# Performance work log

Hardware: AMD Instinct MI355X
Metric: run time of the kernel (lower is better)

The kernel has to match this reference:

```python
import jax, jax.numpy as jnp
import numpy as np

B, S, D, H, FF = 4, 2048, 512, 8, 2048
W = 128  # local attention window size (hardcoded in module)
DH = D // H


def _ln(x, g, b, eps=1e-5):
    m = x.mean(-1, keepdims=True)
    v = ((x - m) ** 2).mean(-1, keepdims=True)
    return (x - m) / jnp.sqrt(v + eps) * g + b


def setup_inputs() -> dict:
    key = jax.random.key(0)
    ks = jax.random.split(key, 10)
    s = 0.02
    return {
        "src": jax.random.normal(ks[0], (B, S, D), jnp.float32),
        # global nn.MultiheadAttention params
        "in_proj_w": jax.random.normal(ks[1], (3 * D, D), jnp.float32) * s,
        "in_proj_b": jnp.zeros((3 * D,), jnp.float32),
        "out_proj_w": jax.random.normal(ks[2], (D, D), jnp.float32) * s,
        "out_proj_b": jnp.zeros((D,), jnp.float32),
        # LocalMHA params (prenorm LN, fused qkv no-bias, out proj no-bias)
        "ln_g": jnp.ones((D,), jnp.float32),
        "ln_b": jnp.zeros((D,), jnp.float32),
        "qkv_w": jax.random.normal(ks[3], (3 * D, D), jnp.float32) * s,
        "to_out_w": jax.random.normal(ks[4], (D, D), jnp.float32) * s,
        # glFusion + FFN + norms
        "gl_w": jax.random.normal(ks[5], (D, 2 * D), jnp.float32) * s,
        "gl_b": jnp.zeros((D,), jnp.float32),
        "norm1_g": jnp.ones((D,), jnp.float32),
        "norm1_b": jnp.zeros((D,), jnp.float32),
        "lin1_w": jax.random.normal(ks[6], (FF, D), jnp.float32) * s,
        "lin1_b": jnp.zeros((FF,), jnp.float32),
        "lin2_w": jax.random.normal(ks[7], (D, FF), jnp.float32) * s,
        "lin2_b": jnp.zeros((D,), jnp.float32),
        "norm2_g": jnp.ones((D,), jnp.float32),
        "norm2_b": jnp.zeros((D,), jnp.float32),
    }


def _forward(src, in_proj_w, in_proj_b, out_proj_w, out_proj_b, ln_g, ln_b,
             qkv_w, to_out_w, gl_w, gl_b, norm1_g, norm1_b,
             lin1_w, lin1_b, lin2_w, lin2_b, norm2_g, norm2_b):
    b, s, d = src.shape
    scale = DH ** -0.5

    def heads(x):  # (b, s, d) -> (b, H, s, DH)
        return x.reshape(b, s, H, DH).transpose(0, 2, 1, 3)

    # ---- global full MHA (no mask) ----
    qkv = src @ in_proj_w.T + in_proj_b
    qg, kg, vg = (heads(t) for t in jnp.split(qkv, 3, axis=-1))
    att = jax.nn.softmax(jnp.einsum('bhid,bhjd->bhij', qg, kg) * scale, axis=-1)
    go = jnp.einsum('bhij,bhjd->bhid', att, vg).transpose(0, 2, 1, 3).reshape(b, s, d)
    go = go @ out_proj_w.T + out_proj_b

    # ---- local windowed causal MHA with rotary (window=128, look_backward=1) ----
    x = _ln(src, ln_g, ln_b)  # prenorm
    ql, kl, vl = (heads(t) for t in jnp.split(x @ qkv_w.T, 3, axis=-1))

    pos = jnp.arange(s)
    inv_freq = 1.0 / (10000.0 ** (jnp.arange(0, DH, 2, dtype=jnp.float32) / DH))
    freqs = pos[:, None].astype(jnp.float32) * inv_freq[None, :]
    emb = jnp.concatenate([freqs, freqs], axis=-1)  # (s, DH)
    cos, sin = jnp.cos(emb), jnp.sin(emb)

    def rope(t):
        h = DH // 2
        t1, t2 = t[..., :h], t[..., h:]
        return t * cos + jnp.concatenate([-t2, t1], axis=-1) * sin

    ql, kl = rope(ql), rope(kl)
    ql = ql * scale

    nw = s // W
    qw = ql.reshape(b, H, nw, W, DH)
    kw = kl.reshape(b, H, nw, W, DH)
    vw = vl.reshape(b, H, nw, W, DH)

    def look_back(t):  # concat previous window with current: (b,H,nw,2W,DH)
        prev = jnp.pad(t, ((0, 0), (0, 0), (1, 0), (0, 0), (0, 0)))[:, :, :-1]
        return jnp.concatenate([prev, t], axis=3)

    bk, bv = look_back(kw), look_back(vw)

    qpos = pos.reshape(nw, W)
    kpos = jnp.concatenate(
        [jnp.concatenate([jnp.full((1, W), -1, pos.dtype), qpos[:-1]], axis=0), qpos],
        axis=1)  # (nw, 2W)
    mask = (kpos[:, None, :] >= 0) & (kpos[:, None, :] <= qpos[:, :, None])  # (nw,W,2W)

    sc = jnp.einsum('bhnid,bhnjd->bhnij', qw, bk)
    sc = jnp.where(mask, sc, jnp.finfo(sc.dtype).min)
    at = jax.nn.softmax(sc, axis=-1)
    lo = jnp.einsum('bhnij,bhnjd->bhnid', at, bv).reshape(b, H, s, DH)
    lo = lo.transpose(0, 2, 1, 3).reshape(b, s, d) @ to_out_w.T

    # ---- fuse global+local, residual, norms, FFN ----
    src2 = jnp.concatenate([go, lo], axis=-1) @ gl_w.T + gl_b
    h1 = _ln(src + src2, norm1_g, norm1_b)
    ff = jax.nn.relu(h1 @ lin1_w.T + lin1_b) @ lin2_w.T + lin2_b
    return _ln(h1 + ff, norm2_g, norm2_b)


def reference(src, in_proj_w, in_proj_b, out_proj_w, out_proj_b, ln_g, ln_b,
              qkv_w, to_out_w, gl_w, gl_b, norm1_g, norm1_b,
              lin1_w, lin1_b, lin2_w, lin2_b, norm2_g, norm2_b):
    return _forward(src, in_proj_w, in_proj_b, out_proj_w, out_proj_b, ln_g, ln_b,
                    qkv_w, to_out_w, gl_w, gl_b, norm1_g, norm1_b,
                    lin1_w, lin1_b, lin2_w, lin2_b, norm2_g, norm2_b)
```

## Files before the change

### kernel.cpp

```cpp
#include <hip/hip_runtime.h>
#include <math.h>

#define B_  4
#define S_  2048
#define D_  512
#define H_  8
#define FF_ 2048
#define W_  128
#define DH_ 64
#define TRD (3*D_)
#define MR_ (B_*S_)
#define LDO_ 1024

typedef __attribute__((ext_vector_type(8)))  short short8;
typedef __attribute__((ext_vector_type(4)))  float f32x4;
typedef __attribute__((ext_vector_type(16))) float f32x16;

__device__ __forceinline__ short f2bf(float f) {
    unsigned u = __float_as_uint(f);
    unsigned r = (u + 0x7fff + ((u >> 16) & 1)) >> 16;
    return (short)r;
}
__device__ __forceinline__ float bf2f(ushort u) {
    return __uint_as_float(((unsigned)u) << 16);
}
__device__ __forceinline__ unsigned pack_bf_trunc(float f0, float f1) {
    return __builtin_amdgcn_perm(__float_as_uint(f1), __float_as_uint(f0), 0x07060302u);
}
__device__ __forceinline__ void gload_lds16(const ushort* g, short* l) {
    __builtin_amdgcn_global_load_lds(
        (const __attribute__((address_space(1))) void*)g,
        (__attribute__((address_space(3))) void*)l, 16, 0, 0);
}

struct CvtJobs { const float* s[8]; ushort* d[8]; int n[8]; };

__global__ __launch_bounds__(256) void cvt_kernel(CvtJobs jobs)
{
    int i4 = (blockIdx.x * 256 + threadIdx.x) * 4;
    #pragma unroll
    for (int j = 0; j < 8; j++) {
        if (i4 < jobs.n[j]) {
            float4 v = *(const float4*)(jobs.s[j] + i4);
            ushort4 o;
            o.x = (ushort)f2bf(v.x); o.y = (ushort)f2bf(v.y);
            o.z = (ushort)f2bf(v.z); o.w = (ushort)f2bf(v.w);
            *(ushort4*)(jobs.d[j] + i4) = o;
        }
    }
}

__global__ __launch_bounds__(256) void gemm_bf16_kernel(
    const ushort* __restrict__ A, int lda,
    const ushort* __restrict__ Wt,
    const float* __restrict__ bias,
    ushort* __restrict__ C, int ldc,
    int K, int relu)
{
    __shared__ short As[128 * 64];
    __shared__ short Bs[64 * 64];
    const int tid  = threadIdx.x;
    const int w    = tid >> 6;
    const int lane = tid & 63;
    const int quad = lane >> 4;
    const int x    = lane & 15;
    const int wr = w >> 1, wc = w & 1;
    const int bm = blockIdx.y * 128;
    const int bn = blockIdx.x * 64;

    const int srow = (lane >> 3);
    const int scol = ((lane & 7) ^ (lane >> 3)) * 8;

    f32x4 acc[4][2];
    #pragma unroll
    for (int i = 0; i < 4; i++)
        #pragma unroll
        for (int j = 0; j < 2; j++) acc[i][j] = (f32x4)0.f;

    for (int k0 = 0; k0 < K; k0 += 64) {
        __syncthreads();
        #pragma unroll
        for (int c = 0; c < 4; c++) {
            const ushort* ga = A + (size_t)(bm + w * 32 + c * 8 + srow) * lda + k0 + scol;
            gload_lds16(ga, &As[(w * 32 + c * 8) * 64]);
        }
        #pragma unroll
        for (int c = 0; c < 2; c++) {
            const ushort* gb = Wt + (size_t)(bn + w * 16 + c * 8 + srow) * K + k0 + scol;
            gload_lds16(gb, &Bs[(w * 16 + c * 8) * 64]);
        }
        __syncthreads();

        #pragma unroll
        for (int kc = 0; kc < 2; kc++) {
            short8 af[4], bf[2];
            int pcg = (kc * 4 + quad) ^ (x & 7);
            #pragma unroll
            for (int i = 0; i < 4; i++)
                af[i] = *(const short8*)&As[(wr * 64 + i * 16 + x) * 64 + pcg * 8];
            #pragma unroll
            for (int j = 0; j < 2; j++)
                bf[j] = *(const short8*)&Bs[(wc * 32 + j * 16 + x) * 64 + pcg * 8];
            #pragma unroll
            for (int i = 0; i < 4; i++)
                #pragma unroll
                for (int j = 0; j < 2; j++)
                    acc[i][j] = __builtin_amdgcn_mfma_f32_16x16x32_bf16(af[i], bf[j], acc[i][j], 0, 0, 0);
        }
    }

    #pragma unroll
    for (int i = 0; i < 4; i++) {
        #pragma unroll
        for (int r = 0; r < 4; r++) {
            size_t row = (size_t)(bm + wr * 64 + i * 16 + quad * 4 + r);
            #pragma unroll
            for (int j = 0; j < 2; j++) {
                int col = bn + wc * 32 + j * 16 + x;
                float v = acc[i][j][r] + (bias ? bias[col] : 0.f);
                if (relu) v = v > 0.f ? v : 0.f;
                C[row * ldc + col] = (ushort)f2bf(v);
            }
        }
    }
}

__device__ __forceinline__ float wave_sum64(float v) {
    #pragma unroll
    for (int off = 32; off > 0; off >>= 1) v += __shfl_xor(v, off, 64);
    return v;
}
__device__ __forceinline__ void load8(const float* p, float* v) {
    *(float4*)&v[0] = *(const float4*)p;
    *(float4*)&v[4] = *(const float4*)(p + 4);
}
__device__ __forceinline__ void load8(const ushort* p, float* v) {
    short8 s = *(const short8*)p;
    #pragma unroll
    for (int i = 0; i < 8; i++) v[i] = bf2f((ushort)s[i]);
}
__device__ __forceinline__ void store8(float* p, const float* v) {
    *(float4*)p       = make_float4(v[0], v[1], v[2], v[3]);
    *(float4*)(p + 4) = make_float4(v[4], v[5], v[6], v[7]);
}
__device__ __forceinline__ void store8(ushort* p, const float* v) {
    short8 s;
    #pragma unroll
    for (int i = 0; i < 8; i++) s[i] = f2bf(v[i]);
    *(short8*)p = s;
}

template <typename TA, typename TB, typename TO>
__global__ __launch_bounds__(256) void addln_kernel(
    const TA* __restrict__ a, const TB* __restrict__ b,
    const float* __restrict__ g, const float* __restrict__ be,
    TO* __restrict__ out)
{
    const int lane = threadIdx.x & 63;
    const int row  = blockIdx.x * 4 + (threadIdx.x >> 6);
    const size_t base = (size_t)row * D_ + lane * 8;
    float v[8];
    load8(a + base, v);
    if (b) {
        float wv[8];
        load8(b + base, wv);
        #pragma unroll
        for (int i = 0; i < 8; i++) v[i] += wv[i];
    }
    float s = 0.f;
    #pragma unroll
    for (int i = 0; i < 8; i++) s += v[i];
    float mean = wave_sum64(s) * (1.0f / 512.0f);
    float vs = 0.f;
    #pragma unroll
    for (int i = 0; i < 8; i++) { float d = v[i] - mean; vs += d * d; }
    float var = wave_sum64(vs) * (1.0f / 512.0f);
    float r = rsqrtf(var + 1e-5f);
    const int c = lane * 8;
    float t[8];
    #pragma unroll
    for (int i = 0; i < 8; i++) t[i] = (v[i] - mean) * r * g[c + i] + be[c + i];
    store8(out + base, t);
}

__global__ __launch_bounds__(256) void transpose_v_kernel(
    const ushort* __restrict__ qkv, ushort* __restrict__ vt)
{
    __shared__ ushort T[64][72];
    const int t  = threadIdx.x;
    const int s0 = blockIdx.x * 64;
    const int bh = blockIdx.y;
    const int b = bh >> 3, h = bh & 7;
    {
        int row = t >> 2, col = (t & 3) * 16;
        const ushort* src = qkv + ((size_t)(b * S_) + s0 + row) * TRD + 2 * D_ + h * DH_ + col;
        *(short8*)&T[row][col]     = *(const short8*)src;
        *(short8*)&T[row][col + 8] = *(const short8*)(src + 8);
    }
    __syncthreads();
    {
        int d = t >> 2, sc = (t & 3) * 16;
        ushort tmp[16];
        #pragma unroll
        for (int k = 0; k < 16; k++) tmp[k] = T[sc + k][d];
        ushort* dst = vt + ((size_t)bh * DH_ + d) * S_ + s0 + sc;
        *(short8*)dst       = *(const short8*)&tmp[0];
        *(short8*)(dst + 8) = *(const short8*)&tmp[8];
    }
}

__global__ __launch_bounds__(256) void transpose512_kernel(
    const ushort* __restrict__ in, ushort* __restrict__ out)
{
    __shared__ ushort T[64][72];
    const int t  = threadIdx.x;
    const int r0 = blockIdx.y * 64, c0 = blockIdx.x * 64;
    {
        int row = t >> 2, col = (t & 3) * 16;
        const ushort* s = in + (size_t)(r0 + row) * 512 + c0 + col;
        *(short8*)&T[row][col]     = *(const short8*)s;
        *(short8*)&T[row][col + 8] = *(const short8*)(s + 8);
    }
    __syncthreads();
    {
        int d = t >> 2, sc = (t & 3) * 16;
        ushort tmp[16];
        #pragma unroll
        for (int k = 0; k < 16; k++) tmp[k] = T[sc + k][d];
        ushort* dptr = out + (size_t)(c0 + d) * 512 + r0 + sc;
        *(short8*)dptr       = *(const short8*)&tmp[0];
        *(short8*)(dptr + 8) = *(const short8*)&tmp[8];
    }
}

__global__ __launch_bounds__(256) void fuse_bias_kernel(
    const float* __restrict__ gl_w, const float* __restrict__ opb,
    const float* __restrict__ gl_b, float* __restrict__ bf)
{
    const int lane = threadIdx.x & 63;
    const int row  = blockIdx.x * 4 + (threadIdx.x >> 6);
    float s = 0.f;
    #pragma unroll
    for (int i = 0; i < 8; i++) {
        int m = lane * 8 + i;
        s += gl_w[(size_t)row * 1024 + m] * opb[m];
    }
    s = wave_sum64(s);
    if (lane == 0) bf[row] = s + gl_b[row];
}

template <int LOCAL>
__global__ __launch_bounds__(256) void attn_kernel(
    const ushort* __restrict__ qkv, const ushort* __restrict__ vt,
    ushort* __restrict__ outp)
{
    __shared__ short KsS[2][64 * 64];
    __shared__ short VtS[2][64 * 64];
    __shared__ float Lw[4][32];

    const int tid  = threadIdx.x;
    const int w    = tid >> 6;
    const int lane = tid & 63;
    const int hl   = lane >> 5;
    const int c    = lane & 31;
    const int ks   = w >> 1;
    const int qh   = w & 1;
    const int bh = blockIdx.y;
    const int b = bh >> 3, h = bh & 7;
    const int qbase = blockIdx.x * 64;
    const int q0 = qbase + qh * 32;
    const size_t bS = (size_t)b * S_;
    const size_t vbase = (size_t)bh * DH_;

    short8 aq[4];
    {
        const ushort* qp = qkv + (bS + q0 + c) * TRD + h * DH_;
        #pragma unroll
        for (int kc = 0; kc < 4; kc++) {
            short8 raw = *(const short8*)(qp + kc * 16 + hl * 8);
            if (LOCAL) aq[kc] = raw;
            else {
                #pragma unroll
                for (int j = 0; j < 8; j++) aq[kc][j] = f2bf(bf2f((ushort)raw[j]) * 0.125f);
            }
        }
    }

    f32x16 ot[2];
    ot[0] = (f32x16)0.f; ot[1] = (f32x16)0.f;
    float lp = 0.f;

    const int NIT = LOCAL ? 2 : (S_ / 64 / 2);
    for (int it = 0; it < NIT; it++) {
        const int tile  = LOCAL ? (ks * 2 + it) : (ks * NIT + it);
        const int kbase = LOCAL ? ((qbase >> 7) * 128 - 128 + tile * 64) : tile * 64;
        const bool active = !LOCAL || (kbase >= 0 && kbase <= qbase + 63);
        __syncthreads();
        if (active) {
            #pragma unroll
            for (int cc = 0; cc < 4; cc++) {
                int row = qh * 32 + cc * 8 + (lane >> 3);
                int cg  = (lane & 7) ^ (lane >> 3);
                gload_lds16(qkv + (bS + kbase + row) * TRD + D_ + h * DH_ + cg * 8,
                            &KsS[ks][(qh * 32 + cc * 8) * 64]);
                gload_lds16(vt + (vbase + row) * S_ + kbase + cg * 8,
                            &VtS[ks][(qh * 32 + cc * 8) * 64]);
            }
        }
        __syncthreads();
        if (!active) continue;
        const bool diag = LOCAL && (kbase == qbase);

        f32x16 e0 = (f32x16)0.f, e1 = (f32x16)0.f;
        #pragma unroll
        for (int kc = 0; kc < 4; kc++) {
            int pcg = (kc * 2 + hl) ^ (c & 7);
            short8 ak0 = *(const short8*)&KsS[ks][c * 64 + pcg * 8];
            e0 = __builtin_amdgcn_mfma_f32_32x32x16_bf16(ak0, aq[kc], e0, 0, 0, 0);
            short8 ak1 = *(const short8*)&KsS[ks][(32 + c) * 64 + pcg * 8];
            e1 = __builtin_amdgcn_mfma_f32_32x32x16_bf16(ak1, aq[kc], e1, 0, 0, 0);
        }

        unsigned pk[2][8];
        const int qi = q0 + c;
        #pragma unroll
        for (int mt = 0; mt < 2; mt++) {
            f32x16& e = mt ? e1 : e0;
            #pragma unroll
            for (int r = 0; r < 16; r++) {
                float p = __expf(e[r]);
                if (diag) {
                    int key = kbase + mt * 32 + (r & 3) + 8 * (r >> 2) + 4 * hl;
                    if (key > qi) p = 0.f;
                }
                e[r] = p;
                lp += p;
            }
            #pragma unroll
            for (int g = 0; g < 8; g++)
                pk[mt][g] = pack_bf_trunc(e[2 * g], e[2 * g + 1]);
        }

        #pragma unroll
        for (int kc = 0; kc < 4; kc++) {
            const int mt = kc >> 1, kp = kc & 1;
            unsigned m0 = pk[mt][4 * kp + 0], m1 = pk[mt][4 * kp + 1];
            unsigned m2 = pk[mt][4 * kp + 2], m3 = pk[mt][4 * kp + 3];
            unsigned s0 = (unsigned)__shfl_xor((int)m0, 32, 64);
            unsigned s1 = (unsigned)__shfl_xor((int)m1, 32, 64);
            unsigned s2 = (unsigned)__shfl_xor((int)m2, 32, 64);
            unsigned s3 = (unsigned)__shfl_xor((int)m3, 32, 64);
            uint4 fd;
            fd.x = hl ? s2 : m0;
            fd.y = hl ? s3 : m1;
            fd.z = hl ? m2 : s0;
            fd.w = hl ? m3 : s1;
            short8 bp = *(short8*)&fd;
            #pragma unroll
            for (int dt = 0; dt < 2; dt++) {
                int row = dt * 32 + c;
                int pcg = (kc * 2 + hl) ^ (c & 7);
                short8 av = *(const short8*)&VtS[ks][row * 64 + pcg * 8];
                ot[dt] = __builtin_amdgcn_mfma_f32_32x32x16_bf16(av, bp, ot[dt], 0, 0, 0);
            }
        }
    }

    lp += __shfl_xor(lp, 32, 64);
    if (hl == 0) Lw[w][c] = lp;
    __syncthreads();

    float* scr = (float*)&KsS[0][0];
    if (w >= 2) {
        float* dst = scr + (w - 2) * 2048;
        #pragma unroll
        for (int dt = 0; dt < 2; dt++)
            #pragma unroll
            for (int r = 0; r < 16; r++)
                dst[(dt * 16 + r) * 64 + lane] = ot[dt][r];
    }
    __syncthreads();
    if (w < 2) {
        const float* srcp = scr + w * 2048;
        #pragma unroll
        for (int dt = 0; dt < 2; dt++)
            #pragma unroll
            for (int r = 0; r < 16; r++)
                ot[dt][r] += srcp[(dt * 16 + r) * 64 + lane];
        float inv = 1.0f / (Lw[w][c] + Lw[w + 2][c]);

        short* tr = (short*)&VtS[0][0] + w * 2304;
        #pragma unroll
        for (int dt = 0; dt < 2; dt++)
            #pragma unroll
            for (int rq = 0; rq < 4; rq++) {
                uint2 pkv;
                pkv.x = pack_bf_trunc(ot[dt][rq * 4 + 0] * inv, ot[dt][rq * 4 + 1] * inv);
                pkv.y = pack_bf_trunc(ot[dt][rq * 4 + 2] * inv, ot[dt][rq * 4 + 3] * inv);
                *(uint2*)&tr[c * 72 + dt * 32 + 8 * rq + 4 * hl] = pkv;
            }
        asm volatile("s_waitcnt lgkmcnt(0)" ::: "memory");
        __builtin_amdgcn_wave_barrier();
        {
            int q  = lane >> 1;
            int d0 = (lane & 1) * 32;
            short8 v0 = *(const short8*)&tr[q * 72 + d0];
            short8 v1 = *(const short8*)&tr[q * 72 + d0 + 8];
            short8 v2 = *(const short8*)&tr[q * 72 + d0 + 16];
            short8 v3 = *(const short8*)&tr[q * 72 + d0 + 24];
            ushort* op = outp + (bS + q0 + q) * LDO_ + h * DH_ + d0;
            *(short8*)(op)      = v0;
            *(short8*)(op + 8)  = v1;
            *(short8*)(op + 16) = v2;
            *(short8*)(op + 24) = v3;
        }
    }
}

__global__ __launch_bounds__(256) void rope_kernel(ushort* __restrict__ qkv)
{
    int idx = blockIdx.x * 256 + threadIdx.x;
    int d  = idx & 31;
    int h  = (idx >> 5) & 7;
    int bs = idx >> 8;
    int pos = bs & (S_ - 1);
    float inv_freq = exp2f(-(float)d * (2.0f / 64.0f) * 13.287712379549449f);
    float ang = (float)pos * inv_freq;
    float sn, cs;
    sincosf(ang, &sn, &cs);
    ushort* base = qkv + (size_t)bs * TRD + h * DH_;
    float q1 = bf2f(base[d]), q2 = bf2f(base[d + 32]);
    base[d]      = (ushort)f2bf((q1 * cs - q2 * sn) * 0.125f);
    base[d + 32] = (ushort)f2bf((q2 * cs + q1 * sn) * 0.125f);
    ushort* kb = base + D_;
    float k1 = bf2f(kb[d]), k2 = bf2f(kb[d + 32]);
    kb[d]      = (ushort)f2bf(k1 * cs - k2 * sn);
    kb[d + 32] = (ushort)f2bf(k2 * cs + k1 * sn);
}

extern "C" void kernel_launch(void* const* d_in, const int* in_sizes, int n_in,
                              void* d_out, int out_size, void* d_ws, size_t ws_size,
                              hipStream_t stream)
{
    (void)in_sizes; (void)n_in; (void)out_size; (void)ws_size;
    const float* src        = (const float*)d_in[0];
    const float* in_proj_w  = (const float*)d_in[1];
    const float* in_proj_b  = (const float*)d_in[2];
    const float* out_proj_w = (const float*)d_in[3];
    const float* out_proj_b = (const float*)d_in[4];
    const float* ln_g       = (const float*)d_in[5];
    const float* ln_b       = (const float*)d_in[6];
    const float* qkv_w      = (const float*)d_in[7];
    const float* to_out_w   = (const float*)d_in[8];
    const float* gl_w       = (const float*)d_in[9];
    const float* gl_b       = (const float*)d_in[10];
    const float* norm1_g    = (const float*)d_in[11];
    const float* norm1_b    = (const float*)d_in[12];
    const float* lin1_w     = (const float*)d_in[13];
    const float* lin1_b     = (const float*)d_in[14];
    const float* lin2_w     = (const float*)d_in[15];
    const float* lin2_b     = (const float*)d_in[16];
    const float* norm2_g    = (const float*)d_in[17];
    const float* norm2_b    = (const float*)d_in[18];
    float* out = (float*)d_out;

    ushort* ws16   = (ushort*)d_ws;
    ushort* src_bf = ws16;
    ushort* wi_bf  = src_bf + (size_t)MR_ * D_;
    ushort* wq_bf  = wi_bf  + TRD * D_;
    ushort* wo_bf  = wq_bf  + TRD * D_;
    ushort* wt_bf  = wo_bf  + D_ * D_;
    ushort* wg_bf  = wt_bf  + D_ * D_;
    ushort* w1_bf  = wg_bf  + D_ * 2 * D_;
    ushort* w2_bf  = w1_bf  + FF_ * D_;
    ushort* opwT   = w2_bf  + D_ * FF_;
    ushort* towT   = opwT   + D_ * D_;
    ushort* wcat   = towT   + D_ * D_;
    ushort* buf1   = wcat   + D_ * 2 * D_;
    ushort* h1b    = buf1   + (size_t)MR_ * D_;
    ushort* buf0   = h1b    + (size_t)MR_ * D_;
    ushort* cat    = buf0   + (size_t)MR_ * TRD;
    ushort* vtb    = cat    + (size_t)MR_ * 2 * D_;
    float*  bfuse  = (float*)(vtb + (size_t)MR_ * D_);
    ushort* ff1    = buf0;

    dim3 blk256(256);

    CvtJobs jobs;
    jobs.s[0] = src;        jobs.d[0] = src_bf; jobs.n[0] = MR_ * D_;
    jobs.s[1] = in_proj_w;  jobs.d[1] = wi_bf;  jobs.n[1] = TRD * D_;
    jobs.s[2] = qkv_w;      jobs.d[2] = wq_bf;  jobs.n[2] = TRD * D_;
    jobs.s[3] = out_proj_w; jobs.d[3] = wo_bf;  jobs.n[3] = D_ * D_;
    jobs.s[4] = to_out_w;   jobs.d[4] = wt_bf;  jobs.n[4] = D_ * D_;
    jobs.s[5] = gl_w;       jobs.d[5] = wg_bf;  jobs.n[5] = D_ * 2 * D_;
    jobs.s[6] = lin1_w;     jobs.d[6] = w1_bf;  jobs.n[6] = FF_ * D_;
    jobs.s[7] = lin2_w;     jobs.d[7] = w2_bf;  jobs.n[7] = D_ * FF_;
    cvt_kernel<<<dim3((MR_ * D_ / 4 + 255) / 256), blk256, 0, stream>>>(jobs);

    transpose512_kernel<<<dim3(8, 8), blk256, 0, stream>>>(wo_bf, opwT);
    transpose512_kernel<<<dim3(8, 8), blk256, 0, stream>>>(wt_bf, towT);
    gemm_bf16_kernel<<<dim3(D_ / 64, D_ / 128), blk256, 0, stream>>>(
        wg_bf, 2 * D_, opwT, nullptr, wcat, 2 * D_, D_, 0);
    gemm_bf16_kernel<<<dim3(D_ / 64, D_ / 128), blk256, 0, stream>>>(
        wg_bf + D_, 2 * D_, towT, nullptr, wcat + D_, 2 * D_, D_, 0);
    fuse_bias_kernel<<<dim3(D_ / 4), blk256, 0, stream>>>(gl_w, out_proj_b, gl_b, bfuse);

    gemm_bf16_kernel<<<dim3(TRD / 64, MR_ / 128), blk256, 0, stream>>>(
        src_bf, D_, wi_bf, in_proj_b, buf0, TRD, D_, 0);
    transpose_v_kernel<<<dim3(S_ / 64, B_ * H_), blk256, 0, stream>>>(buf0, vtb);
    attn_kernel<0><<<dim3(S_ / 64, B_ * H_), blk256, 0, stream>>>(buf0, vtb, cat);
    addln_kernel<float, float, ushort><<<dim3(MR_ / 4), blk256, 0, stream>>>(
        src, (const float*)nullptr, ln_g, ln_b, buf1);
    gemm_bf16_kernel<<<dim3(TRD / 64, MR_ / 128), blk256, 0, stream>>>(
        buf1, D_, wq_bf, nullptr, buf0, TRD, D_, 0);
    transpose_v_kernel<<<dim3(S_ / 64, B_ * H_), blk256, 0, stream>>>(buf0, vtb);
    rope_kernel<<<dim3((B_ * S_ * H_ * 32) / 256), blk256, 0, stream>>>(buf0);
    attn_kernel<1><<<dim3(S_ / 64, B_ * H_), blk256, 0, stream>>>(buf0, vtb, cat + D_);
    gemm_bf16_kernel<<<dim3(D_ / 64, MR_ / 128), blk256, 0, stream>>>(
        cat, 2 * D_, wcat, bfuse, buf1, D_, 2 * D_, 0);
    addln_kernel<float, ushort, ushort><<<dim3(MR_ / 4), blk256, 0, stream>>>(
        src, buf1, norm1_g, norm1_b, h1b);
    gemm_bf16_kernel<<<dim3(FF_ / 64, MR_ / 128), blk256, 0, stream>>>(
        h1b, D_, w1_bf, lin1_b, ff1, FF_, D_, 1);
    gemm_bf16_kernel<<<dim3(D_ / 64, MR_ / 128), blk256, 0, stream>>>(
        ff1, FF_, w2_bf, lin2_b, buf1, D_, FF_, 0);
    addln_kernel<ushort, ushort, float><<<dim3(MR_ / 4), blk256, 0, stream>>>(
        h1b, buf1, norm2_g, norm2_b, out);
}
```

Baseline: 440.2 us.

## Fuse V transpose into QKV GEMM, merge attention launches, split-K narrow GEMMs

The QKV GEMM epilogue now writes V straight into a transposed per-head layout, which removes the separate transpose kernels. The global and local attention passes run as one launch indexed by blockIdx.z. The softmax switches to exp2 with the scale folded into Q, and the P-operand shuffle is replaced by direct packing. The two narrow-output GEMMs (the fused out-projection and lin2) use a 2-way split-K that writes fp32 partials, and a new LayerNorm kernel sums those partials with the bias. RoPE is vectorised to 8 elements per thread. The split-K partials add fp32 memory traffic in exchange for more blocks in flight.

```diff
diff --git a/kernel.cpp b/kernel.cpp
--- a/kernel.cpp
+++ b/kernel.cpp
@@ -10,7 +10,8 @@
 #define DH_ 64
 #define TRD (3*D_)
 #define MR_ (B_*S_)
-#define LDO_ 1024
+#define QKLD 1024
+#define SCQ 0.18033688011112042f
 
 typedef __attribute__((ext_vector_type(8)))  short short8;
 typedef __attribute__((ext_vector_type(4)))  float f32x4;
@@ -55,6 +56,7 @@
     const ushort* __restrict__ Wt,
     const float* __restrict__ bias,
     ushort* __restrict__ C, int ldc,
+    ushort* __restrict__ vt,
     int K, int relu)
 {
     __shared__ short As[128 * 64];
@@ -109,20 +111,121 @@
         }
     }
 
-    #pragma unroll
-    for (int i = 0; i < 4; i++) {
+    if (vt) {
+        #pragma unroll
+        for (int i = 0; i < 4; i++) {
+            int rowbase = bm + wr * 64 + i * 16 + quad * 4;
+            #pragma unroll
+            for (int j = 0; j < 2; j++) {
+                int col = bn + wc * 32 + j * 16 + x;
+                float bv = bias ? bias[col] : 0.f;
+                if (col < 1024) {
+                    #pragma unroll
+                    for (int r = 0; r < 4; r++)
+                        C[(size_t)(rowbase + r) * QKLD + col] = (ushort)f2bf(acc[i][j][r] + bv);
+                } else {
+                    int cv = col - 1024, hh = cv >> 6, dd = cv & 63;
+                    int bb = rowbase >> 11, ss = rowbase & 2047;
+                    int quadp = ((quad & 1) << 1) | (quad >> 1);
+                    int sp = (ss & ~15) | (quadp << 2);
+                    ushort4 p4;
+                    p4.x = (ushort)f2bf(acc[i][j][0] + bv);
+                    p4.y = (ushort)f2bf(acc[i][j][1] + bv);
+                    p4.z = (ushort)f2bf(acc[i][j][2] + bv);
+                    p4.w = (ushort)f2bf(acc[i][j][3] + bv);
+                    *(ushort4*)(vt + ((size_t)((bb * 8 + hh) * 64 + dd)) * S_ + sp) = p4;
+                }
+            }
+        }
+    } else {
+        #pragma unroll
+        for (int i = 0; i < 4; i++) {
+            #pragma unroll
+            for (int r = 0; r < 4; r++) {
+                size_t row = (size_t)(bm + wr * 64 + i * 16 + quad * 4 + r);
+                #pragma unroll
+                for (int j = 0; j < 2; j++) {
+                    int col = bn + wc * 32 + j * 16 + x;
+                    float v = acc[i][j][r] + (bias ? bias[col] : 0.f);
+                    if (relu) v = v > 0.f ? v : 0.f;
+                    C[row * ldc + col] = (ushort)f2bf(v);
+                }
+            }
+        }
+    }
+}
+
+__global__ __launch_bounds__(256) void gemm_bf16_splitk_kernel(
+    const ushort* __restrict__ A, int lda,
+    const ushort* __restrict__ Wt,
+    float* __restrict__ P, int K)
+{
+    __shared__ short As[128 * 64];
+    __shared__ short Bs[64 * 64];
+    const int tid  = threadIdx.x;
+    const int w    = tid >> 6;
+    const int lane = tid & 63;
+    const int quad = lane >> 4;
+    const int x    = lane & 15;
+    const int wr = w >> 1, wc = w & 1;
+    const int bm = blockIdx.y * 128;
+    const int bn = blockIdx.x * 64;
+    const int kh = K >> 1;
+    const int kbeg = blockIdx.z * kh;
+    float* dst = P + (size_t)blockIdx.z * MR_ * D_;
+
+    const int srow = (lane >> 3);
+    const int scol = ((lane & 7) ^ (lane >> 3)) * 8;
+
+    f32x4 acc[4][2];
+    #pragma unroll
+    for (int i = 0; i < 4; i++)
+        #pragma unroll
+        for (int j = 0; j < 2; j++) acc[i][j] = (f32x4)0.f;
+
+    for (int k0 = kbeg; k0 < kbeg + kh; k0 += 64) {
+        __syncthreads();
+        #pragma unroll
+        for (int c = 0; c < 4; c++) {
+            const ushort* ga = A + (size_t)(bm + w * 32 + c * 8 + srow) * lda + k0 + scol;
+            gload_lds16(ga, &As[(w * 32 + c * 8) * 64]);
+        }
+        #pragma unroll
+        for (int c = 0; c < 2; c++) {
+            const ushort* gb = Wt + (size_t)(bn + w * 16 + c * 8 + srow) * K + k0 + scol;
+            gload_lds16(gb, &Bs[(w * 16 + c * 8) * 64]);
+        }
+        __syncthreads();
+
+        #pragma unroll
+        for (int kc = 0; kc < 2; kc++) {
+            short8 af[4], bf[2];
+            int pcg = (kc * 4 + quad) ^ (x & 7);
+            #pragma unroll
+            for (int i = 0; i < 4; i++)
+                af[i] = *(const short8*)&As[(wr * 64 + i * 16 + x) * 64 + pcg * 8];
+            #pragma unroll
+            for (int j = 0; j < 2; j++)
+                bf[j] = *(const short8*)&Bs[(wc * 32 + j * 16 + x) * 64 + pcg * 8];
+            #pragma unroll
+            for (int i = 0; i < 4; i++)
+                #pragma unroll
+                for (int j = 0; j < 2; j++)
+                    acc[i][j] = __builtin_amdgcn_mfma_f32_16x16x32_bf16(af[i], bf[j], acc[i][j], 0, 0, 0);
+        }
+    }
+
+    #pragma unroll
+    for (int i = 0; i < 4; i++)
         #pragma unroll
         for (int r = 0; r < 4; r++) {
             size_t row = (size_t)(bm + wr * 64 + i * 16 + quad * 4 + r);
             #pragma unroll
             for (int j = 0; j < 2; j++) {
                 int col = bn + wc * 32 + j * 16 + x;
-                float v = acc[i][j][r] + (bias ? bias[col] : 0.f);
-                if (relu) v = v > 0.f ? v : 0.f;
-                C[row * ldc + col] = (ushort)f2bf(v);
-            }
-        }
-    }
+                dst[row * D_ + col] = acc[i][j][r];
+            }
+        }
 }
 
 __device__ __forceinline__ float wave_sum64(float v) {
@@ -149,24 +252,8 @@
     for (int i = 0; i < 8; i++) s[i] = f2bf(v[i]);
     *(short8*)p = s;
 }
-
-template <typename TA, typename TB, typename TO>
-__global__ __launch_bounds__(256) void addln_kernel(
-    const TA* __restrict__ a, const TB* __restrict__ b,
-    const float* __restrict__ g, const float* __restrict__ be,
-    TO* __restrict__ out)
-{
-    const int lane = threadIdx.x & 63;
-    const int row  = blockIdx.x * 4 + (threadIdx.x >> 6);
-    const size_t base = (size_t)row * D_ + lane * 8;
-    float v[8];
-    load8(a + base, v);
-    if (b) {
-        float wv[8];
-        load8(b + base, wv);
-        #pragma unroll
-        for (int i = 0; i < 8; i++) v[i] += wv[i];
-    }
+__device__ __forceinline__ void ln_core(float* v, int lane,
+    const float* g, const float* be, float* t) {
     float s = 0.f;
     #pragma unroll
     for (int i = 0; i < 8; i++) s += v[i];
@@ -177,36 +264,45 @@
     float var = wave_sum64(vs) * (1.0f / 512.0f);
     float r = rsqrtf(var + 1e-5f);
     const int c = lane * 8;
-    float t[8];
     #pragma unroll
     for (int i = 0; i < 8; i++) t[i] = (v[i] - mean) * r * g[c + i] + be[c + i];
+}
+
+template <typename TA, typename TO>
+__global__ __launch_bounds__(256) void addln_kernel(
+    const TA* __restrict__ a,
+    const float* __restrict__ g, const float* __restrict__ be,
+    TO* __restrict__ out)
+{
+    const int lane = threadIdx.x & 63;
+    const int row  = blockIdx.x * 4 + (threadIdx.x >> 6);
+    const size_t base = (size_t)row * D_ + lane * 8;
+    float v[8], t[8];
+    load8(a + base, v);
+    ln_core(v, lane, g, be, t);
     store8(out + base, t);
 }
 
-__global__ __launch_bounds__(256) void transpose_v_kernel(
-    const ushort* __restrict__ qkv, ushort* __restrict__ vt)
-{
-    __shared__ ushort T[64][72];
-    const int t  = threadIdx.x;
-    const int s0 = blockIdx.x * 64;
-    const int bh = blockIdx.y;
-    const int b = bh >> 3, h = bh & 7;
-    {
-        int row = t >> 2, col = (t & 3) * 16;
-        const ushort* src = qkv + ((size_t)(b * S_) + s0 + row) * TRD + 2 * D_ + h * DH_ + col;
-        *(short8*)&T[row][col]     = *(const short8*)src;
-        *(short8*)&T[row][col + 8] = *(const short8*)(src + 8);
-    }
-    __syncthreads();
-    {
-        int d = t >> 2, sc = (t & 3) * 16;
-        ushort tmp[16];
-        #pragma unroll
-        for (int k = 0; k < 16; k++) tmp[k] = T[sc + k][d];
-        ushort* dst = vt + ((size_t)bh * DH_ + d) * S_ + s0 + sc;
-        *(short8*)dst       = *(const short8*)&tmp[0];
-        *(short8*)(dst + 8) = *(const short8*)&tmp[8];
-    }
+template <typename TA, typename TO>
+__global__ __launch_bounds__(256) void ln_split_kernel(
+    const TA* __restrict__ a,
+    const float* __restrict__ p0, const float* __restrict__ p1,
+    const float* __restrict__ bias,
+    const float* __restrict__ g, const float* __restrict__ be,
+    TO* __restrict__ out)
+{
+    const int lane = threadIdx.x & 63;
+    const int row  = blockIdx.x * 4 + (threadIdx.x >> 6);
+    const size_t base = (size_t)row * D_ + lane * 8;
+    float v[8], w0[8], w1[8], t[8];
+    load8(a + base, v);
+    load8(p0 + base, w0);
+    load8(p1 + base, w1);
+    const int c = lane * 8;
+    #pragma unroll
+    for (int i = 0; i < 8; i++) v[i] += w0[i] + w1[i] + bias[c + i];
+    ln_core(v, lane, g, be, t);
+    store8(out + base, t);
 }
 
 __global__ __launch_bounds__(256) void transpose512_kernel(
@@ -249,14 +345,47 @@
     if (lane == 0) bf[row] = s + gl_b[row];
 }
 
-template <int LOCAL>
+__global__ __launch_bounds__(256) void rope_kernel(ushort* __restrict__ qk)
+{
+    int idx = blockIdx.x * 256 + threadIdx.x;
+    int d8 = idx & 3;
+    int h  = (idx >> 2) & 7;
+    int bs = idx >> 5;
+    int pos = bs & (S_ - 1);
+    ushort* base = qk + (size_t)bs * QKLD + h * 64 + d8 * 8;
+    float q1[8], q2[8], k1[8], k2[8];
+    load8(base, q1);       load8(base + 32, q2);
+    load8(base + 512, k1); load8(base + 544, k2);
+    float oq1[8], oq2[8], ok1[8], ok2[8];
+    #pragma unroll
+    for (int i = 0; i < 8; i++) {
+        int d = d8 * 8 + i;
+        float inv_freq = exp2f(-(float)d * (2.0f / 64.0f) * 13.287712379549449f);
+        float ang = (float)pos * inv_freq;
+        float sn, cs;
+        __sincosf(ang, &sn, &cs);
+        oq1[i] = (q1[i] * cs - q2[i] * sn) * SCQ;
+        oq2[i] = (q2[i] * cs + q1[i] * sn) * SCQ;
+        ok1[i] = k1[i] * cs - k2[i] * sn;
+        ok2[i] = k2[i] * cs + k1[i] * sn;
+    }
+    store8(base, oq1);       store8(base + 32, oq2);
+    store8(base + 512, ok1); store8(base + 544, ok2);
+}
+
 __global__ __launch_bounds__(256) void attn_kernel(
-    const ushort* __restrict__ qkv, const ushort* __restrict__ vt,
-    ushort* __restrict__ outp)
+    const ushort* __restrict__ qkG, const ushort* __restrict__ vtG,
+    const ushort* __restrict__ qkL, const ushort* __restrict__ vtL,
+    ushort* __restrict__ cat)
 {
     __shared__ short KsS[2][64 * 64];
     __shared__ short VtS[2][64 * 64];
     __shared__ float Lw[4][32];
+
+    const int LOCAL = blockIdx.z;
+    const ushort* qk = LOCAL ? qkL : qkG;
+    const ushort* vt = LOCAL ? vtL : vtG;
+    ushort* outp = cat + (LOCAL ? D_ : 0);
 
     const int tid  = threadIdx.x;
     const int w    = tid >> 6;
@@ -274,14 +403,14 @@
 
     short8 aq[4];
     {
-        const ushort* qp = qkv + (bS + q0 + c) * TRD + h * DH_;
+        const ushort* qp = qk + (bS + q0 + c) * QKLD + h * 64;
         #pragma unroll
         for (int kc = 0; kc < 4; kc++) {
             short8 raw = *(const short8*)(qp + kc * 16 + hl * 8);
             if (LOCAL) aq[kc] = raw;
             else {
                 #pragma unroll
-                for (int j = 0; j < 8; j++) aq[kc][j] = f2bf(bf2f((ushort)raw[j]) * 0.125f);
+                for (int j = 0; j < 8; j++) aq[kc][j] = f2bf(bf2f((ushort)raw[j]) * SCQ);
             }
         }
     }
@@ -290,9 +419,9 @@
     ot[0] = (f32x16)0.f; ot[1] = (f32x16)0.f;
     float lp = 0.f;
 
-    const int NIT = LOCAL ? 2 : (S_ / 64 / 2);
+    const int NIT = LOCAL ? 2 : 16;
     for (int it = 0; it < NIT; it++) {
-        const int tile  = LOCAL ? (ks * 2 + it) : (ks * NIT + it);
+        const int tile  = ks * NIT + it;
         const int kbase = LOCAL ? ((qbase >> 7) * 128 - 128 + tile * 64) : tile * 64;
         const bool active = !LOCAL || (kbase >= 0 && kbase <= qbase + 63);
         __syncthreads();
@@ -301,7 +430,7 @@
             for (int cc = 0; cc < 4; cc++) {
                 int row = qh * 32 + cc * 8 + (lane >> 3);
                 int cg  = (lane & 7) ^ (lane >> 3);
-                gload_lds16(qkv + (bS + kbase + row) * TRD + D_ + h * DH_ + cg * 8,
+                gload_lds16(qk + (bS + kbase + row) * QKLD + 512 + h * 64 + cg * 8,
                             &KsS[ks][(qh * 32 + cc * 8) * 64]);
                 gload_lds16(vt + (vbase + row) * S_ + kbase + cg * 8,
                             &VtS[ks][(qh * 32 + cc * 8) * 64]);
@@ -321,14 +450,13 @@
             e1 = __builtin_amdgcn_mfma_f32_32x32x16_bf16(ak1, aq[kc], e1, 0, 0, 0);
         }
 
-        unsigned pk[2][8];
         const int qi = q0 + c;
         #pragma unroll
         for (int mt = 0; mt < 2; mt++) {
             f32x16& e = mt ? e1 : e0;
             #pragma unroll
             for (int r = 0; r < 16; r++) {
-                float p = __expf(e[r]);
+                float p = exp2f(e[r]);
                 if (diag) {
                     int key = kbase + mt * 32 + (r & 3) + 8 * (r >> 2) + 4 * hl;
                     if (key > qi) p = 0.f;
@@ -336,30 +464,22 @@
                 e[r] = p;
                 lp += p;
             }
-            #pragma unroll
-            for (int g = 0; g < 8; g++)
-                pk[mt][g] = pack_bf_trunc(e[2 * g], e[2 * g + 1]);
-        }
-
-        #pragma unroll
-        for (int kc = 0; kc < 4; kc++) {
-            const int mt = kc >> 1, kp = kc & 1;
-            unsigned m0 = pk[mt][4 * kp + 0], m1 = pk[mt][4 * kp + 1];
-            unsigned m2 = pk[mt][4 * kp + 2], m3 = pk[mt][4 * kp + 3];
-            unsigned s0 = (unsigned)__shfl_xor((int)m0, 32, 64);
-            unsigned s1 = (unsigned)__shfl_xor((int)m1, 32, 64);
-            unsigned s2 = (unsigned)__shfl_xor((int)m2, 32, 64);
-            unsigned s3 = (unsigned)__shfl_xor((int)m3, 32, 64);
-            uint4 fd;
-            fd.x = hl ? s2 : m0;
-            fd.y = hl ? s3 : m1;
-            fd.z = hl ? m2 : s0;
-            fd.w = hl ? m3 : s1;
-            short8 bp = *(short8*)&fd;
+        }
+
+        #pragma unroll
+        for (int t = 0; t < 4; t++) {
+            const f32x16& e = (t < 2) ? e0 : e1;
+            const int rb = 8 * (t & 1);
+            uint4 u;
+            u.x = pack_bf_trunc(e[rb + 0], e[rb + 1]);
+            u.y = pack_bf_trunc(e[rb + 2], e[rb + 3]);
+            u.z = pack_bf_trunc(e[rb + 4], e[rb + 5]);
+            u.w = pack_bf_trunc(e[rb + 6], e[rb + 7]);
+            short8 bp = *(short8*)&u;
             #pragma unroll
             for (int dt = 0; dt < 2; dt++) {
                 int row = dt * 32 + c;
-                int pcg = (kc * 2 + hl) ^ (c & 7);
+                int pcg = (t * 2 + hl) ^ (c & 7);
                 short8 av = *(const short8*)&VtS[ks][row * 64 + pcg * 8];
                 ot[dt] = __builtin_amdgcn_mfma_f32_32x32x16_bf16(av, bp, ot[dt], 0, 0, 0);
             }
@@ -408,34 +528,13 @@
             short8 v1 = *(const short8*)&tr[q * 72 + d0 + 8];
             short8 v2 = *(const short8*)&tr[q * 72 + d0 + 16];
             short8 v3 = *(const short8*)&tr[q * 72 + d0 + 24];
-            ushort* op = outp + (bS + q0 + q) * LDO_ + h * DH_ + d0;
+            ushort* op = outp + (bS + q0 + q) * 1024 + h * 64 + d0;
             *(short8*)(op)      = v0;
             *(short8*)(op + 8)  = v1;
             *(short8*)(op + 16) = v2;
             *(short8*)(op + 24) = v3;
         }
     }
-}
-
-__global__ __launch_bounds__(256) void rope_kernel(ushort* __restrict__ qkv)
-{
-    int idx = blockIdx.x * 256 + threadIdx.x;
-    int d  = idx & 31;
-    int h  = (idx >> 5) & 7;
-    int bs = idx >> 8;
-    int pos = bs & (S_ - 1);
-    float inv_freq = exp2f(-(float)d * (2.0f / 64.0f) * 13.287712379549449f);
-    float ang = (float)pos * inv_freq;
-    float sn, cs;
-    sincosf(ang, &sn, &cs);
-    ushort* base = qkv + (size_t)bs * TRD + h * DH_;
-    float q1 = bf2f(base[d]), q2 = bf2f(base[d + 32]);
-    base[d]      = (ushort)f2bf((q1 * cs - q2 * sn) * 0.125f);
-    base[d + 32] = (ushort)f2bf((q2 * cs + q1 * sn) * 0.125f);
-    ushort* kb = base + D_;
-    float k1 = bf2f(kb[d]), k2 = bf2f(kb[d + 32]);
-    kb[d]      = (ushort)f2bf(k1 * cs - k2 * sn);
-    kb[d + 32] = (ushort)f2bf(k2 * cs + k1 * sn);
 }
 
 extern "C" void kernel_launch(void* const* d_in, const int* in_sizes, int n_in,
@@ -476,13 +575,16 @@
     ushort* opwT   = w2_bf  + D_ * FF_;
     ushort* towT   = opwT   + D_ * D_;
     ushort* wcat   = towT   + D_ * D_;
-    ushort* buf1   = wcat   + D_ * 2 * D_;
-    ushort* h1b    = buf1   + (size_t)MR_ * D_;
-    ushort* buf0   = h1b    + (size_t)MR_ * D_;
-    ushort* cat    = buf0   + (size_t)MR_ * TRD;
-    ushort* vtb    = cat    + (size_t)MR_ * 2 * D_;
-    float*  bfuse  = (float*)(vtb + (size_t)MR_ * D_);
-    ushort* ff1    = buf0;
+    float*  bfuse  = (float*)(wcat + D_ * 2 * D_);
+    ushort* buf1   = (ushort*)(bfuse + D_);
+    ushort* h1b    = buf1 + (size_t)MR_ * D_;
+    ushort* qkG    = h1b  + (size_t)MR_ * D_;
+    ushort* vtg    = qkG  + (size_t)MR_ * QKLD;
+    ushort* qkL    = vtg  + (size_t)MR_ * D_;
+    ushort* vtl    = qkL  + (size_t)MR_ * QKLD;
+    ushort* cat    = vtl  + (size_t)MR_ * D_;
+    float*  part   = (float*)qkG;
+    ushort* ff1    = qkL + (size_t)MR_ * D_;
 
     dim3 blk256(256);
 
@@ -495,35 +597,33 @@
     jobs.s[5] = gl_w;       jobs.d[5] = wg_bf;  jobs.n[5] = D_ * 2 * D_;
     jobs.s[6] = lin1_w;     jobs.d[6] = w1_bf;  jobs.n[6] = FF_ * D_;
     jobs.s[7] = lin2_w;     jobs.d[7] = w2_bf;  jobs.n[7] = D_ * FF_;
-    cvt_kernel<<<dim3((MR_ * D_ / 4 + 255) / 256), blk256, 0, stream>>>(jobs);
+    cvt_kernel<<<dim3(4096), blk256, 0, stream>>>(jobs);
 
     transpose512_kernel<<<dim3(8, 8), blk256, 0, stream>>>(wo_bf, opwT);
     transpose512_kernel<<<dim3(8, 8), blk256, 0, stream>>>(wt_bf, towT);
-    gemm_bf16_kernel<<<dim3(D_ / 64, D_ / 128), blk256, 0, stream>>>(
-        wg_bf, 2 * D_, opwT, nullptr, wcat, 2 * D_, D_, 0);
-    gemm_bf16_kernel<<<dim3(D_ / 64, D_ / 128), blk256, 0, stream>>>(
-        wg_bf + D_, 2 * D_, towT, nullptr, wcat + D_, 2 * D_, D_, 0);
+    gemm_bf16_kernel<<<dim3(8, 4), blk256, 0, stream>>>(
+        wg_bf, 2 * D_, opwT, nullptr, wcat, 2 * D_, nullptr, D_, 0);
+    gemm_bf16_kernel<<<dim3(8, 4), blk256, 0, stream>>>(
+        wg_bf + D_, 2 * D_, towT, nullptr, wcat + D_, 2 * D_, nullptr, D_, 0);
     fuse_bias_kernel<<<dim3(D_ / 4), blk256, 0, stream>>>(gl_w, out_proj_b, gl_b, bfuse);
 
     gemm_bf16_kernel<<<dim3(TRD / 64, MR_ / 128), blk256, 0, stream>>>(
-        src_bf, D_, wi_bf, in_proj_b, buf0, TRD, D_, 0);
-    transpose_v_kernel<<<dim3(S_ / 64, B_ * H_), blk256, 0, stream>>>(buf0, vtb);
-    attn_kernel<0><<<dim3(S_ / 64, B_ * H_), blk256, 0, stream>>>(buf0, vtb, cat);
-    addln_kernel<float, float, ushort><<<dim3(MR_ / 4), blk256, 0, stream>>>(
-        src, (const float*)nullptr, ln_g, ln_b, buf1);
+        src_bf, D_, wi_bf, in_proj_b, qkG, QKLD, vtg, D_, 0);
+    addln_kernel<float, ushort><<<dim3(MR_ / 4), blk256, 0, stream>>>(
+        src, ln_g, ln_b, buf1);
     gemm_bf16_kernel<<<dim3(TRD / 64, MR_ / 128), blk256, 0, stream>>>(
-        buf1, D_, wq_bf, nullptr, buf0, TRD, D_, 0);
-    transpose_v_kernel<<<dim3(S_ / 64, B_ * H_), blk256, 0, stream>>>(buf0, vtb);
-    rope_kernel<<<dim3((B_ * S_ * H_ * 32) / 256), blk256, 0, stream>>>(buf0);
-    attn_kernel<1><<<dim3(S_ / 64, B_ * H_), blk256, 0, stream>>>(buf0, vtb, cat + D_);
-    gemm_bf16_kernel<<<dim3(D_ / 64, MR_ / 128), blk256, 0, stream>>>(
-        cat, 2 * D_, wcat, bfuse, buf1, D_, 2 * D_, 0);
-    addln_kernel<float, ushort, ushort><<<dim3(MR_ / 4), blk256, 0, stream>>>(
-        src, buf1, norm1_g, norm1_b, h1b);
+        buf1, D_, wq_bf, nullptr, qkL, QKLD, vtl, D_, 0);
+    rope_kernel<<<dim3((B_ * S_ * H_ * 4) / 256), blk256, 0, stream>>>(qkL);
+    attn_kernel<<<dim3(S_ / 64, B_ * H_, 2), blk256, 0, stream>>>(
+        qkG, vtg, qkL, vtl, cat);
+    gemm_bf16_splitk_kernel<<<dim3(D_ / 64, MR_ / 128, 2), blk256, 0, stream>>>(
+        cat, 2 * D_, wcat, part, 2 * D_);
+    ln_split_kernel<float, ushort><<<dim3(MR_ / 4), blk256, 0, stream>>>(
+        src, part, part + (size_t)MR_ * D_, bfuse, norm1_g, norm1_b, h1b);
     gemm_bf16_kernel<<<dim3(FF_ / 64, MR_ / 128), blk256, 0, stream>>>(
-        h1b, D_, w1_bf, lin1_b, ff1, FF_, D_, 1);
-    gemm_bf16_kernel<<<dim3(D_ / 64, MR_ / 128), blk256, 0, stream>>>(
-        ff1, FF_, w2_bf, lin2_b, buf1, D_, FF_, 0);
-    addln_kernel<ushort, ushort, float><<<dim3(MR_ / 4), blk256, 0, stream>>>(
-        h1b, buf1, norm2_g, norm2_b, out);
-}
+        h1b, D_, w1_bf, lin1_b, ff1, FF_, nullptr, D_, 1);
+    gemm_bf16_splitk_kernel<<<dim3(D_ / 64, MR_ / 128, 2), blk256, 0, stream>>>(
+        ff1, FF_, w2_bf, part, FF_);
+    ln_split_kernel<ushort, float><<<dim3(MR_ / 4), blk256, 0, stream>>>(
+        h1b, part, part + (size_t)MR_ * D_, lin2_b, norm2_g, norm2_b, out);
+}
```

Measured after the change: 407.3 us. 7.5% less time.
